# Kernel optimization log

Hardware: AMD Instinct MI355X
Metric: run time of the kernel (lower is better)

## Reference

```python
import jax, jax.numpy as jnp
import numpy as np
from jax import lax

BETA = 0.25


def setup_inputs() -> dict:
    key = jax.random.key(0)
    k1, k2 = jax.random.split(key)
    z = jax.random.normal(k1, (16, 64, 32, 32), dtype=jnp.float32)
    # codebook initialized uniform(-1/K, 1/K) in the original; small random is fine for a baseline
    weight = jax.random.uniform(k2, (8192, 64), dtype=jnp.float32, minval=-1.0 / 8192, maxval=1.0 / 8192)
    return {"z": z, "weight": weight}


def reference(z, weight):
    B, D, H, W = z.shape  # D == embedding_dim
    zf = jnp.transpose(z, (0, 2, 3, 1)).reshape(-1, D)  # [N, D]
    # squared L2 distances: ||z||^2 - 2 z.W^T + ||W||^2  -> [N, K]
    dist = (jnp.sum(zf * zf, axis=1, keepdims=True)
            - 2.0 * jnp.matmul(zf, weight.T)
            + jnp.sum(weight * weight, axis=1))
    idx = jnp.argmin(dist, axis=1)  # [N]
    qe = weight[idx]  # [N, D] gather
    quantized = jnp.transpose(qe.reshape(B, H, W, D), (0, 3, 1, 2))  # back to NCHW
    codebook_loss = jnp.mean((qe - lax.stop_gradient(zf)) ** 2)
    commitment_loss = BETA * jnp.mean((zf - lax.stop_gradient(qe)) ** 2)
    # straight-through estimator
    quantized_st = z + lax.stop_gradient(quantized - z)
    return quantized_st, commitment_loss, codebook_loss
```

## Files before the change

kernel.cpp:

```cpp
#include <hip/hip_runtime.h>
#include <hip/hip_bf16.h>
#include <stdint.h>


typedef __bf16 bf16x8 __attribute__((ext_vector_type(8)));
typedef float f32x16 __attribute__((ext_vector_type(16)));

__global__ __launch_bounds__(256)
void vq_prep(const float* __restrict__ w, __bf16* __restrict__ wbf,
             float* __restrict__ wnneg, unsigned* __restrict__ cand)
{
  const int i = blockIdx.x * 256 + threadIdx.x;
  const float v = w[i];
  wbf[i] = (__bf16)v;
  float s = v * v;
#pragma unroll
  for (int m = 1; m < 64; m <<= 1) s += __shfl_xor(s, m);
  if ((threadIdx.x & 63) == 0) wnneg[i >> 6] = -0.5f * s;
  if (blockIdx.x < 64) cand[i] = 0;
}

__global__ __launch_bounds__(512, 2)
void vq_argmax(const float* __restrict__ z, const __bf16* __restrict__ wbf,
               const float* __restrict__ wnneg, unsigned* __restrict__ cand)
{
  __shared__ __align__(16) char bufs[3][16384];
  __shared__ __align__(16) float wnl[1024];
  const int t = threadIdx.x;
  const int lane = t & 63, wv = t >> 6;
  const int hi = lane >> 5, hi4 = hi << 2, rA = lane & 31;
  const int ksp = blockIdx.x & 7, zgrp = blockIdx.x >> 3;
  const int kbase = ksp << 10;
  const int b = zgrp >> 2;
  const int hw0 = (zgrp & 3) << 8;
  const int ch = wv >> 1, rg = wv & 1;

  ((float2*)wnl)[t] = ((const float2*)(wnneg + kbase))[t];
  asm volatile("s_waitcnt lgkmcnt(0)" ::: "memory");

  auto STAGE = [&](int s) {
    char* buf = &bufs[s % 3][0];
    if (s < 4) {
      const char* src = (const char*)z
          + (((size_t)((b << 6) + (s << 4) + wv)) << 12) + (hw0 << 2) + (lane << 4);
      __builtin_amdgcn_global_load_lds(
          (const __attribute__((address_space(1))) void*)src,
          (__attribute__((address_space(3))) void*)(buf + (wv << 10)), 16, 0, 0);
      __builtin_amdgcn_global_load_lds(
          (const __attribute__((address_space(1))) void*)(src + ((size_t)8 << 12)),
          (__attribute__((address_space(3))) void*)(buf + 8192 + (wv << 10)), 16, 0, 0);
    } else {
      const int st = s - 4;
      const int tt = t & 255;
      const int row = tt >> 3, slot = (tt & 7) ^ (row & 7);
      const int q0 = t >> 8, q1 = q0 + 2;
      const char* wb = (const char*)wbf;
      const char* s0 = wb + (((size_t)(kbase + (q0 << 8) + (st << 5) + row)) << 7) + (slot << 4);
      const char* s1 = wb + (((size_t)(kbase + (q1 << 8) + (st << 5) + row)) << 7) + (slot << 4);
      char* d0 = buf + (q0 << 12) + ((wv & 3) << 10);
      char* d1 = buf + (q1 << 12) + ((wv & 3) << 10);
      __builtin_amdgcn_global_load_lds((const __attribute__((address_space(1))) void*)s0,
          (__attribute__((address_space(3))) void*)d0, 16, 0, 0);
      __builtin_amdgcn_global_load_lds((const __attribute__((address_space(1))) void*)s1,
          (__attribute__((address_space(3))) void*)d1, 16, 0, 0);
    }
  };

  STAGE(0); STAGE(1);

  bf16x8 zf[4][4];
#pragma unroll
  for (int c = 0; c < 4; ++c) {
    asm volatile("s_waitcnt vmcnt(2)" ::: "memory");
    asm volatile("s_barrier" ::: "memory");
    const float* zp = (const float*)(&bufs[c % 3][0] + (hi << 13));
#pragma unroll
    for (int nt = 0; nt < 4; ++nt) {
      const int nl = (rg << 7) + (nt << 5) + rA;
      bf16x8 zv;
#pragma unroll
      for (int j = 0; j < 8; ++j) zv[j] = (__bf16)zp[(j << 8) + nl];
      zf[nt][c] = zv;
    }
    STAGE(c + 2);
  }

  float bestraw[4] = {-3.0e38f, -3.0e38f, -3.0e38f, -3.0e38f};
  float bestpk[4]  = {-3.0e38f, -3.0e38f, -3.0e38f, -3.0e38f};

#pragma unroll 1
  for (int i = 4; i < 12; ++i) {
    if (i < 11) asm volatile("s_waitcnt vmcnt(2)" ::: "memory");
    else        asm volatile("s_waitcnt vmcnt(0)" ::: "memory");
    asm volatile("s_barrier" ::: "memory");
    const int st = i - 4;
    const char* tb = &bufs[i % 3][0] + (ch << 12);

    bf16x8 af[4];
#pragma unroll
    for (int ks = 0; ks < 4; ++ks) {
      const int c16 = (ks << 1) + hi;
      af[ks] = *(const bf16x8*)(tb + (rA << 7) + ((c16 ^ (rA & 7)) << 4));
    }

    const int kloc = (ch << 8) + (st << 5);
    f32x16 acc[4];
#pragma unroll
    for (int nt = 0; nt < 4; ++nt) {
      const float4 q0 = *(const float4*)(wnl + kloc + hi4);
      const float4 q1 = *(const float4*)(wnl + kloc + 8 + hi4);
      const float4 q2 = *(const float4*)(wnl + kloc + 16 + hi4);
      const float4 q3 = *(const float4*)(wnl + kloc + 24 + hi4);
      acc[nt] = (f32x16){q0.x, q0.y, q0.z, q0.w, q1.x, q1.y, q1.z, q1.w,
                         q2.x, q2.y, q2.z, q2.w, q3.x, q3.y, q3.z, q3.w};
    }
#pragma unroll
    for (int ks = 0; ks < 4; ++ks) {
#pragma unroll
      for (int nt = 0; nt < 4; ++nt)
        acc[nt] = __builtin_amdgcn_mfma_f32_32x32x16_bf16(af[ks], zf[nt][ks], acc[nt], 0, 0, 0);
    }

    const unsigned kidx = (unsigned)(kbase + kloc + hi4);
#pragma unroll
    for (int nt = 0; nt < 4; ++nt) {
      const f32x16 a = acc[nt];
      float t0 = fmaxf(fmaxf(a[0], a[1]), a[2]);
      float t1 = fmaxf(fmaxf(a[3], a[4]), a[5]);
      float t2 = fmaxf(fmaxf(a[6], a[7]), a[8]);
      float t3 = fmaxf(fmaxf(a[9], a[10]), a[11]);
      float t4 = fmaxf(fmaxf(a[12], a[13]), a[14]);
      const float m = fmaxf(fmaxf(fmaxf(t0, t1), t2), fmaxf(fmaxf(t3, t4), a[15]));
      if (__any(m > bestraw[nt])) {
        float pk[16];
#pragma unroll
        for (int r = 0; r < 16; ++r) {
          const unsigned pat = (unsigned)((r & 3) + ((r >> 2) << 3));
          pk[r] = __uint_as_float((__float_as_uint(a[r]) & 0xFFFFE000u) | pat);
        }
        float p0 = fmaxf(fmaxf(pk[0], pk[1]), pk[2]);
        float p1 = fmaxf(fmaxf(pk[3], pk[4]), pk[5]);
        float p2 = fmaxf(fmaxf(pk[6], pk[7]), pk[8]);
        float p3 = fmaxf(fmaxf(pk[9], pk[10]), pk[11]);
        float p4 = fmaxf(fmaxf(pk[12], pk[13]), pk[14]);
        const float mx = fmaxf(fmaxf(fmaxf(p0, p1), p2), fmaxf(fmaxf(p3, p4), pk[15]));
        bestpk[nt] = fmaxf(bestpk[nt], __uint_as_float(__float_as_uint(mx) | kidx));
      }
      bestraw[nt] = fmaxf(bestraw[nt], m);
    }
    if (i < 10) STAGE(i + 2);
  }

#pragma unroll
  for (int nt = 0; nt < 4; ++nt) {
    const float bp = fmaxf(bestpk[nt], __shfl_down(bestpk[nt], 32));
    if (lane < 32) {
      const unsigned u = __float_as_uint(bp);
      const unsigned sv = (u & 0x80000000u) ? ~u : (u | 0x80000000u);
      atomicMax(cand + ((zgrp << 8) + (rg << 7) + (nt << 5) + lane), sv);
    }
  }
}

__global__ __launch_bounds__(256)
void vq_gather(const unsigned* __restrict__ cand, const float* __restrict__ w,
               const float* __restrict__ z, float* __restrict__ out,
               float* __restrict__ partials)
{
  const int t = threadIdx.x;
  const int lane = t & 63;
  const int wv = t >> 6;
  const int n = blockIdx.x * 64 + lane;
  const unsigned s = cand[n];
  const unsigned u = (s & 0x80000000u) ? (s & 0x7FFFFFFFu) : ~s;
  const int idx = (int)(u & 8191u);
  const int b = n >> 10, hw = n & 1023;
  const size_t zb = ((size_t)b << 16) | (unsigned)hw;
  const float4* wr = (const float4*)(w + ((size_t)idx << 6));
  float sq = 0.0f;
#pragma unroll
  for (int q = 0; q < 4; ++q) {
    const float4 wvv = wr[(wv << 2) + q];
    const int d0 = (wv << 4) + (q << 2);
#pragma unroll
    for (int j = 0; j < 4; ++j) {
      const float wc = (j == 0) ? wvv.x : (j == 1) ? wvv.y : (j == 2) ? wvv.z : wvv.w;
      const size_t o = zb + ((size_t)(d0 + j) << 10);
      const float df = wc - z[o];
      sq += df * df;
      out[o] = wc;
    }
  }
#pragma unroll
  for (int m = 1; m < 64; m <<= 1) sq += __shfl_xor(sq, m);
  __shared__ float ps[4];
  if (lane == 0) ps[wv] = sq;
  __syncthreads();
  if (t == 0) partials[blockIdx.x] = ps[0] + ps[1] + ps[2] + ps[3];
}

__global__ __launch_bounds__(256)
void vq_finalize(const float* __restrict__ partials, float* __restrict__ out)
{
  const int t = threadIdx.x;
  float v = partials[t];
#pragma unroll
  for (int m = 1; m < 64; m <<= 1) v += __shfl_xor(v, m);
  __shared__ float ps[4];
  if ((t & 63) == 0) ps[t >> 6] = v;
  __syncthreads();
  if (t == 0) {
    const float mse = (ps[0] + ps[1] + ps[2] + ps[3]) * (1.0f / 1048576.0f);
    out[1048576] = 0.25f * mse;
    out[1048577] = mse;
  }
}

extern "C" void kernel_launch(void* const* d_in, const int* in_sizes, int n_in,
                              void* d_out, int out_size, void* d_ws, size_t ws_size,
                              hipStream_t stream)
{
  (void)in_sizes; (void)n_in; (void)out_size; (void)ws_size;
  const float* z = (const float*)d_in[0];
  const float* w = (const float*)d_in[1];
  float* out = (float*)d_out;
  char* ws = (char*)d_ws;
  unsigned* cand = (unsigned*)ws;
  float* partials = (float*)(ws + 65536);
  __bf16* wbf = (__bf16*)(ws + 66560);
  float* wnneg = (float*)(ws + 66560 + 1048576);

  vq_prep<<<2048, 256, 0, stream>>>(w, wbf, wnneg, cand);
  vq_argmax<<<512, 512, 0, stream>>>(z, wbf, wnneg, cand);
  vq_gather<<<256, 256, 0, stream>>>(cand, w, z, out, partials);
  vq_finalize<<<1, 256, 0, stream>>>(partials, out);
}
```

Baseline: 42.04 us.

## Replace global atomicMax argmin with LDS reduction and per-split stores; drop finalize kernel

Each argmax block now reduces its four codebook-chunk waves through shared memory and writes plain per-split packed maxima. The gather kernel takes the max over the 8 splits itself. That removes the candidate zero-init and the global atomicMax traffic. The finalize kernel is removed: loss partials are accumulated with float atomicAdd into outputs zeroed by the prep kernel, saving one launch. The early-skip branch is also dropped, so every tile packs the full index into the low mantissa bits. This adds unconditional ALU work, and fmaxf on packed negative values changes tie behaviour slightly.

```diff
diff --git a/kernel.cpp b/kernel.cpp
--- a/kernel.cpp
+++ b/kernel.cpp
@@ -8,7 +8,7 @@
 
 __global__ __launch_bounds__(256)
 void vq_prep(const float* __restrict__ w, __bf16* __restrict__ wbf,
-             float* __restrict__ wnneg, unsigned* __restrict__ cand)
+             float* __restrict__ wnneg, float* __restrict__ out)
 {
   const int i = blockIdx.x * 256 + threadIdx.x;
   const float v = w[i];
@@ -17,12 +17,12 @@
 #pragma unroll
   for (int m = 1; m < 64; m <<= 1) s += __shfl_xor(s, m);
   if ((threadIdx.x & 63) == 0) wnneg[i >> 6] = -0.5f * s;
-  if (blockIdx.x < 64) cand[i] = 0;
+  if (blockIdx.x == 0 && threadIdx.x < 2) out[1048576 + threadIdx.x] = 0.0f;
 }
 
 __global__ __launch_bounds__(512, 2)
 void vq_argmax(const float* __restrict__ z, const __bf16* __restrict__ wbf,
-               const float* __restrict__ wnneg, unsigned* __restrict__ cand)
+               const float* __restrict__ wnneg, float* __restrict__ cand)
 {
   __shared__ __align__(16) char bufs[3][16384];
   __shared__ __align__(16) float wnl[1024];
@@ -85,8 +85,7 @@
     STAGE(c + 2);
   }
 
-  float bestraw[4] = {-3.0e38f, -3.0e38f, -3.0e38f, -3.0e38f};
-  float bestpk[4]  = {-3.0e38f, -3.0e38f, -3.0e38f, -3.0e38f};
+  float bestpk[4] = {-3.0e38f, -3.0e38f, -3.0e38f, -3.0e38f};
 
 #pragma unroll 1
   for (int i = 4; i < 12; ++i) {
@@ -121,59 +120,59 @@
         acc[nt] = __builtin_amdgcn_mfma_f32_32x32x16_bf16(af[ks], zf[nt][ks], acc[nt], 0, 0, 0);
     }
 
-    const unsigned kidx = (unsigned)(kbase + kloc + hi4);
+    const unsigned khw = (unsigned)(kbase + kloc + hi4);
 #pragma unroll
     for (int nt = 0; nt < 4; ++nt) {
       const f32x16 a = acc[nt];
-      float t0 = fmaxf(fmaxf(a[0], a[1]), a[2]);
-      float t1 = fmaxf(fmaxf(a[3], a[4]), a[5]);
-      float t2 = fmaxf(fmaxf(a[6], a[7]), a[8]);
-      float t3 = fmaxf(fmaxf(a[9], a[10]), a[11]);
-      float t4 = fmaxf(fmaxf(a[12], a[13]), a[14]);
-      const float m = fmaxf(fmaxf(fmaxf(t0, t1), t2), fmaxf(fmaxf(t3, t4), a[15]));
-      if (__any(m > bestraw[nt])) {
-        float pk[16];
-#pragma unroll
-        for (int r = 0; r < 16; ++r) {
-          const unsigned pat = (unsigned)((r & 3) + ((r >> 2) << 3));
-          pk[r] = __uint_as_float((__float_as_uint(a[r]) & 0xFFFFE000u) | pat);
-        }
-        float p0 = fmaxf(fmaxf(pk[0], pk[1]), pk[2]);
-        float p1 = fmaxf(fmaxf(pk[3], pk[4]), pk[5]);
-        float p2 = fmaxf(fmaxf(pk[6], pk[7]), pk[8]);
-        float p3 = fmaxf(fmaxf(pk[9], pk[10]), pk[11]);
-        float p4 = fmaxf(fmaxf(pk[12], pk[13]), pk[14]);
-        const float mx = fmaxf(fmaxf(fmaxf(p0, p1), p2), fmaxf(fmaxf(p3, p4), pk[15]));
-        bestpk[nt] = fmaxf(bestpk[nt], __uint_as_float(__float_as_uint(mx) | kidx));
+      float pk[16];
+#pragma unroll
+      for (int r = 0; r < 16; ++r) {
+        const unsigned id = khw + (unsigned)((r & 3) + ((r >> 2) << 3));
+        pk[r] = __uint_as_float((__float_as_uint(a[r]) & 0xFFFFE000u) | id);
       }
-      bestraw[nt] = fmaxf(bestraw[nt], m);
+      const float g0 = fmaxf(fmaxf(pk[0], pk[1]), pk[2]);
+      const float g1 = fmaxf(fmaxf(pk[3], pk[4]), pk[5]);
+      const float g2 = fmaxf(fmaxf(pk[6], pk[7]), pk[8]);
+      const float g3 = fmaxf(fmaxf(pk[9], pk[10]), pk[11]);
+      const float g4 = fmaxf(fmaxf(pk[12], pk[13]), pk[14]);
+      const float h0 = fmaxf(fmaxf(g0, g1), g2);
+      const float h1 = fmaxf(fmaxf(g3, g4), pk[15]);
+      bestpk[nt] = fmaxf(bestpk[nt], fmaxf(h0, h1));
     }
     if (i < 10) STAGE(i + 2);
   }
 
-#pragma unroll
-  for (int nt = 0; nt < 4; ++nt) {
-    const float bp = fmaxf(bestpk[nt], __shfl_down(bestpk[nt], 32));
-    if (lane < 32) {
-      const unsigned u = __float_as_uint(bp);
-      const unsigned sv = (u & 0x80000000u) ? ~u : (u | 0x80000000u);
-      atomicMax(cand + ((zgrp << 8) + (rg << 7) + (nt << 5) + lane), sv);
-    }
+  float bp4[4];
+#pragma unroll
+  for (int nt = 0; nt < 4; ++nt)
+    bp4[nt] = fmaxf(bestpk[nt], __shfl_down(bestpk[nt], 32));
+
+  __syncthreads();
+  if (lane < 32) {
+#pragma unroll
+    for (int nt = 0; nt < 4; ++nt)
+      wnl[(ch << 8) + (rg << 7) + (nt << 5) + rA] = bp4[nt];
+  }
+  __syncthreads();
+  if (t < 256) {
+    const float m = fmaxf(fmaxf(wnl[t], wnl[256 + t]),
+                          fmaxf(wnl[512 + t], wnl[768 + t]));
+    cand[(ksp << 14) + (zgrp << 8) + t] = m;
   }
 }
 
 __global__ __launch_bounds__(256)
-void vq_gather(const unsigned* __restrict__ cand, const float* __restrict__ w,
-               const float* __restrict__ z, float* __restrict__ out,
-               float* __restrict__ partials)
+void vq_gather(const float* __restrict__ cand, const float* __restrict__ w,
+               const float* __restrict__ z, float* __restrict__ out)
 {
   const int t = threadIdx.x;
   const int lane = t & 63;
   const int wv = t >> 6;
   const int n = blockIdx.x * 64 + lane;
-  const unsigned s = cand[n];
-  const unsigned u = (s & 0x80000000u) ? (s & 0x7FFFFFFFu) : ~s;
-  const int idx = (int)(u & 8191u);
+  float m = cand[n];
+#pragma unroll
+  for (int k = 1; k < 8; ++k) m = fmaxf(m, cand[(k << 14) + n]);
+  const int idx = (int)(__float_as_uint(m) & 8191u);
   const int b = n >> 10, hw = n & 1023;
   const size_t zb = ((size_t)b << 16) | (unsigned)hw;
   const float4* wr = (const float4*)(w + ((size_t)idx << 6));
@@ -192,27 +191,14 @@
     }
   }
 #pragma unroll
-  for (int m = 1; m < 64; m <<= 1) sq += __shfl_xor(sq, m);
+  for (int s2 = 1; s2 < 64; s2 <<= 1) sq += __shfl_xor(sq, s2);
   __shared__ float ps[4];
   if (lane == 0) ps[wv] = sq;
   __syncthreads();
-  if (t == 0) partials[blockIdx.x] = ps[0] + ps[1] + ps[2] + ps[3];
-}
-
-__global__ __launch_bounds__(256)
-void vq_finalize(const float* __restrict__ partials, float* __restrict__ out)
-{
-  const int t = threadIdx.x;
-  float v = partials[t];
-#pragma unroll
-  for (int m = 1; m < 64; m <<= 1) v += __shfl_xor(v, m);
-  __shared__ float ps[4];
-  if ((t & 63) == 0) ps[t >> 6] = v;
-  __syncthreads();
   if (t == 0) {
-    const float mse = (ps[0] + ps[1] + ps[2] + ps[3]) * (1.0f / 1048576.0f);
-    out[1048576] = 0.25f * mse;
-    out[1048577] = mse;
+    const float s = (ps[0] + ps[1] + ps[2] + ps[3]) * (1.0f / 1048576.0f);
+    atomicAdd(out + 1048576, 0.25f * s);
+    atomicAdd(out + 1048577, s);
   }
 }
 
@@ -225,13 +211,11 @@
   const float* w = (const float*)d_in[1];
   float* out = (float*)d_out;
   char* ws = (char*)d_ws;
-  unsigned* cand = (unsigned*)ws;
-  float* partials = (float*)(ws + 65536);
-  __bf16* wbf = (__bf16*)(ws + 66560);
-  float* wnneg = (float*)(ws + 66560 + 1048576);
-
-  vq_prep<<<2048, 256, 0, stream>>>(w, wbf, wnneg, cand);
+  float* cand = (float*)ws;
+  __bf16* wbf = (__bf16*)(ws + 524288);
+  float* wnneg = (float*)(ws + 524288 + 1048576);
+
+  vq_prep<<<2048, 256, 0, stream>>>(w, wbf, wnneg, out);
   vq_argmax<<<512, 512, 0, stream>>>(z, wbf, wnneg, cand);
-  vq_gather<<<256, 256, 0, stream>>>(cand, w, z, out, partials);
-  vq_finalize<<<1, 256, 0, stream>>>(partials, out);
-}
+  vq_gather<<<256, 256, 0, stream>>>(cand, w, z, out);
+}
```

Result: slower. 44.88 us (+6.7%).
